# Kernel tuning notes

Measured on AMD Instinct MI355X. Metric: run time of the kernel, lower is better.

The kernel has to match this reference:

```python
import math
import jax, jax.numpy as jnp
import numpy as np

B, M, H, K, L = 8, 512, 512, 8, 1024  # batch, block, hidden, heads, span
D = H // K  # head_dim = 64; key/value length = M + L


def _skew(X):
    # shift every row one step right: [B', M, L] -> [B', M, M+L]
    Bp, Mm, Ll = X.shape
    X = jnp.pad(X, ((0, 0), (0, 0), (0, Mm + 1)))
    X = X.reshape(Bp, -1)[:, :-Mm]
    return X.reshape(Bp, Mm, Mm + Ll)


def _unskew(X):
    # reverse of _skew: [B', M, M+L] -> [B', M, L]
    Bp, Mm, Lt = X.shape
    Ll = Lt - Mm
    X = X.reshape(Bp, -1)
    X = jnp.pad(X, ((0, 0), (0, Mm)))
    X = X.reshape(Bp, Mm, Mm + Ll + 1)
    return X[:, :, :Ll]


def _heads(x):
    # [B, T, K*D] -> [B*K, T, D]
    b, t, _ = x.shape
    return x.reshape(b, t, K, D).transpose(0, 2, 1, 3).reshape(b * K, t, D)


def setup_inputs() -> dict:
    key0 = jax.random.key(0)
    ks = jax.random.split(key0, 8)
    s = 1.0 / math.sqrt(H)
    return {
        "query": jax.random.normal(ks[0], (B, M, H), jnp.float32),
        "key": jax.random.normal(ks[1], (B, M + L, H), jnp.float32),
        "value": jax.random.normal(ks[2], (B, M + L, H), jnp.float32),
        "key_pe": jax.random.normal(ks[3], (1, D, L), jnp.float32),
        "Wq": jax.random.normal(ks[4], (H, H), jnp.float32) * s,
        "Wk": jax.random.normal(ks[5], (H, H), jnp.float32) * s,
        "Wv": jax.random.normal(ks[6], (H, H), jnp.float32) * s,
        "Wo": jax.random.normal(ks[7], (H, H), jnp.float32) * s,
    }


def reference(query, key, value, key_pe, Wq, Wk, Wv, Wo):
    q = _heads(query @ Wq.T)   # [B*K, M, D]
    k = _heads(key @ Wk.T)     # [B*K, M+L, D]
    v = _heads(value @ Wv.T)   # [B*K, M+L, D]

    attn_cont = jnp.einsum('bmd,bnd->bmn', q, k)       # [B*K, M, M+L]
    attn_cont = _unskew(attn_cont)                      # [B*K, M, L]
    attn_pos = jnp.einsum('bmd,dl->bml', q, key_pe[0])  # [B*K, M, L]
    attn = jax.nn.softmax((attn_cont + attn_pos) / math.sqrt(D), axis=-1)

    attn_sk = _skew(attn)                               # [B*K, M, M+L]
    out = jnp.einsum('bmn,bnd->bmd', attn_sk, v)        # [B*K, M, D]
    out = out.reshape(B, K, M, D).transpose(0, 2, 1, 3).reshape(B, M, K * D)
    return out @ Wo.T
```

## Files before the change

### kernel.cpp

```cpp
#include <hip/hip_runtime.h>
#include <hip/hip_bf16.h>
#include <cstddef>
#include <math.h>


#define HDIM 512
#define MQ 512
#define NK 1536
#define LSPAN 1024
#define SHIFT 5.0f

typedef _Float16 f16_t;
typedef f16_t f16x8 __attribute__((ext_vector_type(8)));
typedef f16_t f16x4 __attribute__((ext_vector_type(4)));
typedef float f32x4 __attribute__((ext_vector_type(4)));

#define MFMA16F(a, b, c) __builtin_amdgcn_mfma_f32_16x16x32_f16((a), (b), (c), 0, 0, 0)

__device__ __forceinline__ void async_cp16(const void* g, void* l) {
  __builtin_amdgcn_global_load_lds((const __attribute__((address_space(1))) void*)g,
                                   (__attribute__((address_space(3))) void*)l, 16, 0, 0);
}

__global__ void cvt_qkv(const float* __restrict__ q, const float* __restrict__ k,
                        const float* __restrict__ v, f16_t* __restrict__ q16,
                        f16_t* __restrict__ k16, f16_t* __restrict__ v16) {
  int y = blockIdx.y;
  const float* s = (y == 0) ? q : (y == 1) ? k : v;
  f16_t* d = (y == 0) ? q16 : (y == 1) ? k16 : v16;
  int n4 = (y == 0) ? 524288 : 1572864;
  int i = blockIdx.x * 256 + threadIdx.x;
  if (i >= n4) return;
  float4 x = ((const float4*)s)[i];
  f16x4 o;
  o[0] = (f16_t)x.x; o[1] = (f16_t)x.y; o[2] = (f16_t)x.z; o[3] = (f16_t)x.w;
  ((f16x4*)d)[i] = o;
}

__global__ void prep_w(const float* __restrict__ Wq, const float* __restrict__ Wk,
                       const float* __restrict__ Wv, const float* __restrict__ Wo,
                       const float* __restrict__ pe,
                       f16_t* __restrict__ wq, f16_t* __restrict__ wk,
                       f16_t* __restrict__ wv, f16_t* __restrict__ wo,
                       f16_t* __restrict__ pet) {
  int i = blockIdx.x * 256 + threadIdx.x;
  if (i < 262144) {
    int seg = i >> 16, j = i & 65535;
    const float* s = (seg == 0) ? Wq : (seg == 1) ? Wk : (seg == 2) ? Wv : Wo;
    f16_t* d = (seg == 0) ? wq : (seg == 1) ? wk : (seg == 2) ? wv : wo;
    float4 x = ((const float4*)s)[j];
    f16x4 o;
    o[0] = (f16_t)x.x; o[1] = (f16_t)x.y; o[2] = (f16_t)x.z; o[3] = (f16_t)x.w;
    ((f16x4*)d)[j] = o;
  } else {
    int j = i - 262144;
    pet[(j & 1023) * 64 + (j >> 10)] = (f16_t)pe[j];
  }
}

__global__ __launch_bounds__(256) void gemm3(
    const f16_t* __restrict__ q16, const f16_t* __restrict__ k16, const f16_t* __restrict__ v16,
    const f16_t* __restrict__ wq, const f16_t* __restrict__ wk, const f16_t* __restrict__ wv,
    f16_t* __restrict__ qo, f16_t* __restrict__ ko, f16_t* __restrict__ vT) {
  __shared__ alignas(16) f16_t As[128 * 64];
  __shared__ alignas(16) f16_t Bs[128 * 64];

  const int bx = blockIdx.x;
  const f16_t *A, *Bm;
  f16_t* C;
  int row0, col0, ldc;
  if (bx < 128) {
    int t = bx;
    A = q16; Bm = wq; C = qo; ldc = HDIM;
    row0 = (t >> 2) * 128; col0 = (t & 3) * 128;
  } else if (bx < 512) {
    int t = bx - 128;
    A = k16; Bm = wk; C = ko; ldc = HDIM;
    row0 = (t >> 2) * 128; col0 = (t & 3) * 128;
  } else {
    int t = bx - 512;
    int b = t / 48, u = t % 48;
    A = wv; Bm = v16 + (size_t)b * NK * HDIM;
    C = vT + (size_t)b * 512 * NK; ldc = NK;
    row0 = (u / 12) * 128; col0 = (u % 12) * 128;
  }

  const int tid = threadIdx.x;
  const int lane = tid & 63, wave = tid >> 6;
  const int quad = lane >> 4, l16 = lane & 15;
  const int wr = (wave & 1) * 64, wc = (wave >> 1) * 64;
  const int rstage = tid >> 3, cstage = tid & 7;

  f32x4 acc[4][4] = {};
  for (int k0 = 0; k0 < HDIM; k0 += 64) {
#pragma unroll
    for (int i = 0; i < 4; ++i) {
      int r = i * 32 + rstage;
      int csw = cstage ^ (r & 7);
      async_cp16(A  + (size_t)(row0 + r) * HDIM + k0 + csw * 8, &As[i * 2048 + wave * 512]);
      async_cp16(Bm + (size_t)(col0 + r) * HDIM + k0 + csw * 8, &Bs[i * 2048 + wave * 512]);
    }
    __syncthreads();
#pragma unroll
    for (int ks = 0; ks < 2; ++ks) {
      f16x8 af[4], bf[4];
#pragma unroll
      for (int i = 0; i < 4; ++i) {
        int rA = wr + i * 16 + l16;
        af[i] = *(const f16x8*)&As[rA * 64 + (((ks * 4 + quad) ^ (rA & 7)) * 8)];
        int rB = wc + i * 16 + l16;
        bf[i] = *(const f16x8*)&Bs[rB * 64 + (((ks * 4 + quad) ^ (rB & 7)) * 8)];
      }
#pragma unroll
      for (int i = 0; i < 4; ++i)
#pragma unroll
        for (int n = 0; n < 4; ++n)
          acc[i][n] = MFMA16F(af[i], bf[n], acc[i][n]);
    }
    __syncthreads();
  }
#pragma unroll
  for (int i = 0; i < 4; ++i)
#pragma unroll
    for (int n = 0; n < 4; ++n)
#pragma unroll
      for (int r = 0; r < 4; ++r)
        C[(size_t)(row0 + wr + i * 16 + quad * 4 + r) * ldc + col0 + wc + n * 16 + l16] =
            (f16_t)acc[i][n][r];
}

__global__ __launch_bounds__(256) void attn2(const f16_t* __restrict__ q,
                                             const f16_t* __restrict__ k,
                                             const f16_t* __restrict__ vT,
                                             const f16_t* __restrict__ pet,
                                             f16_t* __restrict__ Opart,
                                             float* __restrict__ Lpart) {
  __shared__ alignas(16) f16_t Ks[2][4096];
  __shared__ alignas(16) f16_t Vs[4096];
  __shared__ alignas(16) f16_t Tst[4][128][20];
  __shared__ alignas(16) f16_t Ps[4][16][72];

  const int m0 = blockIdx.x * 64;
  const int bh = blockIdx.y;
  const int b = bh >> 3, kh = bh & 7;
  const int z = blockIdx.z;
  const int j0 = z ? 9 : 0, j1 = z ? 16 : 8;
  const int tid = threadIdx.x;
  const int lane = tid & 63, wave = tid >> 6;
  const int quad = lane >> 4, l16 = lane & 15;
  const int sr = wave * 16;
  const int rstage = tid >> 3, cstage = tid & 7;

  f16_t (*Tw)[20] = Tst[wave];
  f16_t (*Pw)[72] = Ps[wave];

  f16x8 qa0, qa1;
  {
    const f16_t* qrow = q + (size_t)(b * MQ + m0 + sr + l16) * HDIM + kh * 64;
    qa0 = *(const f16x8*)(qrow + quad * 8);
    qa1 = *(const f16x8*)(qrow + 32 + quad * 8);
#pragma unroll
    for (int e = 0; e < 8; ++e) {
      qa0[e] = (f16_t)((float)qa0[e] * 0.125f);
      qa1[e] = (f16_t)((float)qa1[e] * 0.125f);
    }
  }

  f16x8 ones;
#pragma unroll
  for (int e = 0; e < 8; ++e) ones[e] = (f16_t)1.0f;

  f32x4 oacc[4] = {};
  f32x4 lacc = {};

  const f16_t* kbh = k + (size_t)b * NK * HDIM + kh * 64;
  const f16_t* vbh = vT + (size_t)(b * 512 + kh * 64) * NK;

  if (z) {
#pragma unroll
    for (int ch = 0; ch < 4; ++ch) {
      int l = 512 + ch * 16 + l16;
      f16x8 s0 = *(const f16x8*)(pet + (size_t)l * 64 + quad * 8);
      f16x8 s1 = *(const f16x8*)(pet + (size_t)l * 64 + 32 + quad * 8);
      f32x4 tt = {};
      tt = MFMA16F(qa0, s0, tt);
      tt = MFMA16F(qa1, s1, tt);
      int sb = l + sr + quad * 4;
#pragma unroll
      for (int r = 0; r < 4; ++r)
        Tw[(sb + r) & 127][quad * 4 + r] = (f16_t)tt[r];
    }
  }

#pragma unroll
  for (int i = 0; i < 2; ++i) {
    int r = i * 32 + rstage;
    int nsrc = m0 + j0 * 64 + r;
    int csw = cstage ^ (r & 7);
    async_cp16(kbh + (size_t)nsrc * HDIM + csw * 8, &Ks[0][i * 2048 + wave * 512]);
  }

  int buf = 0;
  for (int j = j0; j <= j1; ++j, buf ^= 1) {
    __syncthreads();

    f16x8 pb0[4], pb1[4];
    if (j < 16) {
#pragma unroll
      for (int ch = 0; ch < 4; ++ch) {
        int l = j * 64 + ch * 16 + l16;
        pb0[ch] = *(const f16x8*)(pet + (size_t)l * 64 + quad * 8);
        pb1[ch] = *(const f16x8*)(pet + (size_t)l * 64 + 32 + quad * 8);
      }
    }
    {
      int ncol0 = m0 + j * 64;
#pragma unroll
      for (int i = 0; i < 2; ++i) {
        int d = i * 32 + rstage;
        int csw = cstage ^ (d & 7);
        async_cp16(vbh + (size_t)d * NK + ncol0 + csw * 8, &Vs[i * 2048 + wave * 512]);
      }
#pragma unroll
      for (int i = 0; i < 2; ++i) {
        int r = i * 32 + rstage;
        int nsrc = m0 + (j + 1) * 64 + r;
        nsrc = (nsrc < NK) ? nsrc : (NK - 1);
        int csw = cstage ^ (r & 7);
        async_cp16(kbh + (size_t)nsrc * HDIM + csw * 8, &Ks[buf ^ 1][i * 2048 + wave * 512]);
      }
    }
    if (j < 16) {
      const int l0 = j * 64;
#pragma unroll
      for (int ch = 0; ch < 4; ++ch) {
        f32x4 tt = {};
        tt = MFMA16F(qa0, pb0[ch], tt);
        tt = MFMA16F(qa1, pb1[ch], tt);
        int sb = l0 + ch * 16 + l16 + sr + quad * 4;
#pragma unroll
        for (int r = 0; r < 4; ++r)
          Tw[(sb + r) & 127][quad * 4 + r] = (f16_t)tt[r];
      }
    }
    f32x4 sacc[4];
#pragma unroll
    for (int ch = 0; ch < 4; ++ch) {
      int n = ch * 16 + l16;
      const f16_t* kr = &Ks[buf][n * 64];
      f16x8 kb0 = *(const f16x8*)&kr[(quad ^ (n & 7)) * 8];
      f16x8 kb1 = *(const f16x8*)&kr[((quad + 4) ^ (n & 7)) * 8];
      f32x4 s = {};
      s = MFMA16F(qa0, kb0, s);
      s = MFMA16F(qa1, kb1, s);
      sacc[ch] = s;
    }
#pragma unroll
    for (int ch = 0; ch < 4; ++ch) {
      int scol = (j * 64 + ch * 16 + l16) & 127;
      f16x4 tq = *(const f16x4*)&Tw[scol][quad * 4];
#pragma unroll
      for (int r = 0; r < 4; ++r) {
        int il = quad * 4 + r;
        int l = j * 64 + ch * 16 + l16 - sr - il;
        float pe_ = __expf(sacc[ch][r] + (float)tq[r] - SHIFT);
        float pv = (l >= 0 && l < LSPAN) ? pe_ : 0.f;
        Pw[il][ch * 16 + l16] = (f16_t)pv;
      }
    }
    f16x8 pa0 = *(const f16x8*)&Pw[l16][quad * 8];
    f16x8 pa1 = *(const f16x8*)&Pw[l16][32 + quad * 8];
    __builtin_amdgcn_s_waitcnt(0x0F72);
#pragma unroll
    for (int dch = 0; dch < 4; ++dch) {
      int d = dch * 16 + l16;
      const f16_t* vr = &Vs[d * 64];
      f16x8 vb0 = *(const f16x8*)&vr[(quad ^ (d & 7)) * 8];
      f16x8 vb1 = *(const f16x8*)&vr[((quad + 4) ^ (d & 7)) * 8];
      oacc[dch] = MFMA16F(pa0, vb0, oacc[dch]);
      oacc[dch] = MFMA16F(pa1, vb1, oacc[dch]);
    }
    lacc = MFMA16F(pa0, ones, lacc);
    lacc = MFMA16F(pa1, ones, lacc);
  }

  f16_t* Op = Opart + (size_t)z * 2097152;
#pragma unroll
  for (int r = 0; r < 4; ++r) {
    float inv = 1.0f / lacc[r];
    int m = m0 + sr + quad * 4 + r;
#pragma unroll
    for (int dch = 0; dch < 4; ++dch)
      Op[(size_t)(b * MQ + m) * HDIM + kh * 64 + dch * 16 + l16] =
          (f16_t)(oacc[dch][r] * inv);
    if (l16 == 0)
      Lpart[z * 32768 + bh * MQ + m] = lacc[r];
  }
}

__global__ __launch_bounds__(256) void gemm_wo(const f16_t* __restrict__ O0,
                                               const f16_t* __restrict__ O1,
                                               const float* __restrict__ Lpart,
                                               const f16_t* __restrict__ Bw,
                                               float* __restrict__ C) {
  __shared__ alignas(16) f16_t As[128][72];
  __shared__ alignas(16) f16_t Bs[64 * 64];
  const int bx = blockIdx.x;
  const int row0 = (bx >> 3) * 128, col0 = (bx & 7) * 64;
  const int tid = threadIdx.x;
  const int lane = tid & 63, wave = tid >> 6;
  const int quad = lane >> 4, l16 = lane & 15;
  const int wr = (wave & 1) * 64, wc = (wave >> 1) * 32;
  const int rstage = tid >> 3, cstage = tid & 7;
  const int cA8 = (tid & 7) * 8;

  f32x4 acc[4][2] = {};
  for (int k0 = 0; k0 < HDIM; k0 += 64) {
#pragma unroll
    for (int i = 0; i < 2; ++i) {
      int r = i * 32 + rstage;
      int csw = cstage ^ (r & 7);
      async_cp16(Bw + (size_t)(col0 + r) * HDIM + k0 + csw * 8, &Bs[i * 2048 + wave * 512]);
    }
#pragma unroll
    for (int i = 0; i < 4; ++i) {
      int r = i * 32 + rstage;
      int rg = row0 + r;
      int bb = rg >> 9, m = rg & 511;
      int head = (k0 + cA8) >> 6;
      int li = (bb * 8 + head) * MQ + m;
      float l0 = Lpart[li], l1 = Lpart[32768 + li];
      float w0 = l0 / (l0 + l1), w1 = 1.0f - w0;
      f16x8 o0 = *(const f16x8*)(O0 + (size_t)rg * HDIM + k0 + cA8);
      f16x8 o1 = *(const f16x8*)(O1 + (size_t)rg * HDIM + k0 + cA8);
      f16x8 a8;
#pragma unroll
      for (int e = 0; e < 8; ++e)
        a8[e] = (f16_t)((float)o0[e] * w0 + (float)o1[e] * w1);
      *(f16x8*)&As[r][cA8] = a8;
    }
    __syncthreads();
#pragma unroll
    for (int ks = 0; ks < 2; ++ks) {
      f16x8 af[4], bf[2];
#pragma unroll
      for (int i = 0; i < 4; ++i)
        af[i] = *(const f16x8*)&As[wr + i * 16 + l16][(ks * 4 + quad) * 8];
#pragma unroll
      for (int n = 0; n < 2; ++n) {
        int rB = wc + n * 16 + l16;
        bf[n] = *(const f16x8*)&Bs[rB * 64 + (((ks * 4 + quad) ^ (rB & 7)) * 8)];
      }
#pragma unroll
      for (int i = 0; i < 4; ++i)
#pragma unroll
        for (int n = 0; n < 2; ++n)
          acc[i][n] = MFMA16F(af[i], bf[n], acc[i][n]);
    }
    __syncthreads();
  }
#pragma unroll
  for (int i = 0; i < 4; ++i)
#pragma unroll
    for (int n = 0; n < 2; ++n)
#pragma unroll
      for (int r = 0; r < 4; ++r)
        C[(size_t)(row0 + wr + i * 16 + quad * 4 + r) * HDIM + col0 + wc + n * 16 + l16] =
            acc[i][n][r];
}

extern "C" void kernel_launch(void* const* d_in, const int* in_sizes, int n_in,
                              void* d_out, int out_size, void* d_ws, size_t ws_size,
                              hipStream_t stream) {
  const float* query  = (const float*)d_in[0];
  const float* key    = (const float*)d_in[1];
  const float* value  = (const float*)d_in[2];
  const float* key_pe = (const float*)d_in[3];
  const float* Wq     = (const float*)d_in[4];
  const float* Wk     = (const float*)d_in[5];
  const float* Wv     = (const float*)d_in[6];
  const float* Wo     = (const float*)d_in[7];
  float* out = (float*)d_out;

  f16_t* ws = (f16_t*)d_ws;
  f16_t* q16a = ws;
  f16_t* k16a = q16a + 2097152;
  f16_t* v16a = k16a + 6291456;
  f16_t* wq16 = v16a + 6291456;
  f16_t* wk16 = wq16 + 262144;
  f16_t* wv16 = wk16 + 262144;
  f16_t* wo16 = wv16 + 262144;
  f16_t* pet  = wo16 + 262144;
  f16_t* qo   = pet + 65536;
  f16_t* ko   = qo + 2097152;
  f16_t* vTo  = ko + 6291456;
  f16_t* Opart = k16a;
  float* Lpart = (float*)v16a;

  hipLaunchKernelGGL(cvt_qkv, dim3(6144, 3), dim3(256), 0, stream,
                     query, key, value, q16a, k16a, v16a);
  hipLaunchKernelGGL(prep_w, dim3(1280), dim3(256), 0, stream,
                     Wq, Wk, Wv, Wo, key_pe, wq16, wk16, wv16, wo16, pet);
  hipLaunchKernelGGL(gemm3, dim3(896), dim3(256), 0, stream,
                     q16a, k16a, v16a, wq16, wk16, wv16, qo, ko, vTo);
  hipLaunchKernelGGL(attn2, dim3(8, 64, 2), dim3(256), 0, stream,
                     qo, ko, vTo, pet, Opart, Lpart);
  hipLaunchKernelGGL(gemm_wo, dim3(256), dim3(256), 0, stream,
                     Opart, Opart + 2097152, Lpart, wo16, out);
}
```

Baseline: 214.5 us.

## Double-buffer projection GEMMs and merge conversion kernels into one launch

```diff
diff --git a/kernel.cpp b/kernel.cpp
--- a/kernel.cpp
+++ b/kernel.cpp
@@ -22,39 +22,40 @@
                                    (__attribute__((address_space(3))) void*)l, 16, 0, 0);
 }
 
-__global__ void cvt_qkv(const float* __restrict__ q, const float* __restrict__ k,
-                        const float* __restrict__ v, f16_t* __restrict__ q16,
-                        f16_t* __restrict__ k16, f16_t* __restrict__ v16) {
+__global__ void prep_all(const float* __restrict__ q, const float* __restrict__ k,
+                         const float* __restrict__ v,
+                         const float* __restrict__ Wq, const float* __restrict__ Wk,
+                         const float* __restrict__ Wv, const float* __restrict__ Wo,
+                         const float* __restrict__ pe,
+                         f16_t* __restrict__ q16, f16_t* __restrict__ k16,
+                         f16_t* __restrict__ v16,
+                         f16_t* __restrict__ wq, f16_t* __restrict__ wk,
+                         f16_t* __restrict__ wv, f16_t* __restrict__ wo,
+                         f16_t* __restrict__ pet) {
   int y = blockIdx.y;
-  const float* s = (y == 0) ? q : (y == 1) ? k : v;
-  f16_t* d = (y == 0) ? q16 : (y == 1) ? k16 : v16;
-  int n4 = (y == 0) ? 524288 : 1572864;
   int i = blockIdx.x * 256 + threadIdx.x;
-  if (i >= n4) return;
-  float4 x = ((const float4*)s)[i];
-  f16x4 o;
-  o[0] = (f16_t)x.x; o[1] = (f16_t)x.y; o[2] = (f16_t)x.z; o[3] = (f16_t)x.w;
-  ((f16x4*)d)[i] = o;
-}
-
-__global__ void prep_w(const float* __restrict__ Wq, const float* __restrict__ Wk,
-                       const float* __restrict__ Wv, const float* __restrict__ Wo,
-                       const float* __restrict__ pe,
-                       f16_t* __restrict__ wq, f16_t* __restrict__ wk,
-                       f16_t* __restrict__ wv, f16_t* __restrict__ wo,
-                       f16_t* __restrict__ pet) {
-  int i = blockIdx.x * 256 + threadIdx.x;
-  if (i < 262144) {
-    int seg = i >> 16, j = i & 65535;
-    const float* s = (seg == 0) ? Wq : (seg == 1) ? Wk : (seg == 2) ? Wv : Wo;
-    f16_t* d = (seg == 0) ? wq : (seg == 1) ? wk : (seg == 2) ? wv : wo;
-    float4 x = ((const float4*)s)[j];
+  if (y < 3) {
+    const float* s = (y == 0) ? q : (y == 1) ? k : v;
+    f16_t* d = (y == 0) ? q16 : (y == 1) ? k16 : v16;
+    int n4 = (y == 0) ? 524288 : 1572864;
+    if (i >= n4) return;
+    float4 x = ((const float4*)s)[i];
     f16x4 o;
     o[0] = (f16_t)x.x; o[1] = (f16_t)x.y; o[2] = (f16_t)x.z; o[3] = (f16_t)x.w;
-    ((f16x4*)d)[j] = o;
+    ((f16x4*)d)[i] = o;
   } else {
-    int j = i - 262144;
-    pet[(j & 1023) * 64 + (j >> 10)] = (f16_t)pe[j];
+    if (i < 262144) {
+      int seg = i >> 16, j = i & 65535;
+      const float* s = (seg == 0) ? Wq : (seg == 1) ? Wk : (seg == 2) ? Wv : Wo;
+      f16_t* d = (seg == 0) ? wq : (seg == 1) ? wk : (seg == 2) ? wv : wo;
+      float4 x = ((const float4*)s)[j];
+      f16x4 o;
+      o[0] = (f16_t)x.x; o[1] = (f16_t)x.y; o[2] = (f16_t)x.z; o[3] = (f16_t)x.w;
+      ((f16x4*)d)[j] = o;
+    } else if (i < 327680) {
+      int j = i - 262144;
+      pet[(j & 1023) * 64 + (j >> 10)] = (f16_t)pe[j];
+    }
   }
 }
 
@@ -62,8 +63,8 @@
     const f16_t* __restrict__ q16, const f16_t* __restrict__ k16, const f16_t* __restrict__ v16,
     const f16_t* __restrict__ wq, const f16_t* __restrict__ wk, const f16_t* __restrict__ wv,
     f16_t* __restrict__ qo, f16_t* __restrict__ ko, f16_t* __restrict__ vT) {
-  __shared__ alignas(16) f16_t As[128 * 64];
-  __shared__ alignas(16) f16_t Bs[128 * 64];
+  __shared__ alignas(16) f16_t As[2][8192];
+  __shared__ alignas(16) f16_t Bs[2][8192];
 
   const int bx = blockIdx.x;
   const f16_t *A, *Bm;
@@ -91,25 +92,39 @@
   const int wr = (wave & 1) * 64, wc = (wave >> 1) * 64;
   const int rstage = tid >> 3, cstage = tid & 7;
 
+#pragma unroll
+  for (int i = 0; i < 4; ++i) {
+    int r = i * 32 + rstage;
+    int csw = cstage ^ (r & 7);
+    async_cp16(A  + (size_t)(row0 + r) * HDIM + csw * 8, &As[0][i * 2048 + wave * 512]);
+    async_cp16(Bm + (size_t)(col0 + r) * HDIM + csw * 8, &Bs[0][i * 2048 + wave * 512]);
+  }
+
   f32x4 acc[4][4] = {};
-  for (int k0 = 0; k0 < HDIM; k0 += 64) {
-#pragma unroll
-    for (int i = 0; i < 4; ++i) {
-      int r = i * 32 + rstage;
-      int csw = cstage ^ (r & 7);
-      async_cp16(A  + (size_t)(row0 + r) * HDIM + k0 + csw * 8, &As[i * 2048 + wave * 512]);
-      async_cp16(Bm + (size_t)(col0 + r) * HDIM + k0 + csw * 8, &Bs[i * 2048 + wave * 512]);
-    }
+  for (int it = 0; it < 8; ++it) {
+    const int buf = it & 1;
     __syncthreads();
+    if (it + 1 < 8) {
+      int k0 = (it + 1) * 64;
+#pragma unroll
+      for (int i = 0; i < 4; ++i) {
+        int r = i * 32 + rstage;
+        int csw = cstage ^ (r & 7);
+        async_cp16(A  + (size_t)(row0 + r) * HDIM + k0 + csw * 8,
+                   &As[buf ^ 1][i * 2048 + wave * 512]);
+        async_cp16(Bm + (size_t)(col0 + r) * HDIM + k0 + csw * 8,
+                   &Bs[buf ^ 1][i * 2048 + wave * 512]);
+      }
+    }
 #pragma unroll
     for (int ks = 0; ks < 2; ++ks) {
       f16x8 af[4], bf[4];
 #pragma unroll
       for (int i = 0; i < 4; ++i) {
         int rA = wr + i * 16 + l16;
-        af[i] = *(const f16x8*)&As[rA * 64 + (((ks * 4 + quad) ^ (rA & 7)) * 8)];
+        af[i] = *(const f16x8*)&As[buf][rA * 64 + (((ks * 4 + quad) ^ (rA & 7)) * 8)];
         int rB = wc + i * 16 + l16;
-        bf[i] = *(const f16x8*)&Bs[rB * 64 + (((ks * 4 + quad) ^ (rB & 7)) * 8)];
+        bf[i] = *(const f16x8*)&Bs[buf][rB * 64 + (((ks * 4 + quad) ^ (rB & 7)) * 8)];
       }
 #pragma unroll
       for (int i = 0; i < 4; ++i)
@@ -117,7 +132,6 @@
         for (int n = 0; n < 4; ++n)
           acc[i][n] = MFMA16F(af[i], bf[n], acc[i][n]);
     }
-    __syncthreads();
   }
 #pragma unroll
   for (int i = 0; i < 4; ++i)
@@ -303,8 +317,8 @@
                                                const float* __restrict__ Lpart,
                                                const f16_t* __restrict__ Bw,
                                                float* __restrict__ C) {
-  __shared__ alignas(16) f16_t As[128][72];
-  __shared__ alignas(16) f16_t Bs[64 * 64];
+  __shared__ alignas(16) f16_t As[2][128][72];
+  __shared__ alignas(16) f16_t Bs[2][4096];
   const int bx = blockIdx.x;
   const int row0 = (bx >> 3) * 128, col0 = (bx & 7) * 64;
   const int tid = threadIdx.x;
@@ -314,21 +328,14 @@
   const int rstage = tid >> 3, cstage = tid & 7;
   const int cA8 = (tid & 7) * 8;
 
-  f32x4 acc[4][2] = {};
-  for (int k0 = 0; k0 < HDIM; k0 += 64) {
-#pragma unroll
-    for (int i = 0; i < 2; ++i) {
-      int r = i * 32 + rstage;
-      int csw = cstage ^ (r & 7);
-      async_cp16(Bw + (size_t)(col0 + r) * HDIM + k0 + csw * 8, &Bs[i * 2048 + wave * 512]);
-    }
+  f16x8 areg[4];
+  auto loadA = [&](int it) {
+    int k0 = it * 64;
+    int head = (k0 + cA8) >> 6;
 #pragma unroll
     for (int i = 0; i < 4; ++i) {
-      int r = i * 32 + rstage;
-      int rg = row0 + r;
-      int bb = rg >> 9, m = rg & 511;
-      int head = (k0 + cA8) >> 6;
-      int li = (bb * 8 + head) * MQ + m;
+      int rg = row0 + i * 32 + rstage;
+      int li = ((rg >> 9) * 8 + head) * MQ + (rg & 511);
       float l0 = Lpart[li], l1 = Lpart[32768 + li];
       float w0 = l0 / (l0 + l1), w1 = 1.0f - w0;
       f16x8 o0 = *(const f16x8*)(O0 + (size_t)rg * HDIM + k0 + cA8);
@@ -337,19 +344,46 @@
 #pragma unroll
       for (int e = 0; e < 8; ++e)
         a8[e] = (f16_t)((float)o0[e] * w0 + (float)o1[e] * w1);
-      *(f16x8*)&As[r][cA8] = a8;
-    }
+      areg[i] = a8;
+    }
+  };
+
+  loadA(0);
+#pragma unroll
+  for (int i = 0; i < 2; ++i) {
+    int r = i * 32 + rstage;
+    int csw = cstage ^ (r & 7);
+    async_cp16(Bw + (size_t)(col0 + r) * HDIM + csw * 8, &Bs[0][i * 2048 + wave * 512]);
+  }
+#pragma unroll
+  for (int i = 0; i < 4; ++i)
+    *(f16x8*)&As[0][i * 32 + rstage][cA8] = areg[i];
+
+  f32x4 acc[4][2] = {};
+  for (int it = 0; it < 8; ++it) {
+    const int buf = it & 1;
     __syncthreads();
+    if (it + 1 < 8) {
+      int k0 = (it + 1) * 64;
+#pragma unroll
+      for (int i = 0; i < 2; ++i) {
+        int r = i * 32 + rstage;
+        int csw = cstage ^ (r & 7);
+        async_cp16(Bw + (size_t)(col0 + r) * HDIM + k0 + csw * 8,
+                   &Bs[buf ^ 1][i * 2048 + wave * 512]);
+      }
+      loadA(it + 1);
+    }
 #pragma unroll
     for (int ks = 0; ks < 2; ++ks) {
       f16x8 af[4], bf[2];
 #pragma unroll
       for (int i = 0; i < 4; ++i)
-        af[i] = *(const f16x8*)&As[wr + i * 16 + l16][(ks * 4 + quad) * 8];
+        af[i] = *(const f16x8*)&As[buf][wr + i * 16 + l16][(ks * 4 + quad) * 8];
 #pragma unroll
       for (int n = 0; n < 2; ++n) {
         int rB = wc + n * 16 + l16;
-        bf[n] = *(const f16x8*)&Bs[rB * 64 + (((ks * 4 + quad) ^ (rB & 7)) * 8)];
+        bf[n] = *(const f16x8*)&Bs[buf][rB * 64 + (((ks * 4 + quad) ^ (rB & 7)) * 8)];
       }
 #pragma unroll
       for (int i = 0; i < 4; ++i)
@@ -357,7 +391,11 @@
         for (int n = 0; n < 2; ++n)
           acc[i][n] = MFMA16F(af[i], bf[n], acc[i][n]);
     }
-    __syncthreads();
+    if (it + 1 < 8) {
+#pragma unroll
+      for (int i = 0; i < 4; ++i)
+        *(f16x8*)&As[buf ^ 1][i * 32 + rstage][cA8] = areg[i];
+    }
   }
 #pragma unroll
   for (int i = 0; i < 4; ++i)
@@ -397,10 +435,9 @@
   f16_t* Opart = k16a;
   float* Lpart = (float*)v16a;
 
-  hipLaunchKernelGGL(cvt_qkv, dim3(6144, 3), dim3(256), 0, stream,
-                     query, key, value, q16a, k16a, v16a);
-  hipLaunchKernelGGL(prep_w, dim3(1280), dim3(256), 0, stream,
-                     Wq, Wk, Wv, Wo, key_pe, wq16, wk16, wv16, wo16, pet);
+  hipLaunchKernelGGL(prep_all, dim3(6144, 4), dim3(256), 0, stream,
+                     query, key, value, Wq, Wk, Wv, Wo, key_pe,
+                     q16a, k16a, v16a, wq16, wk16, wv16, wo16, pet);
   hipLaunchKernelGGL(gemm3, dim3(896), dim3(256), 0, stream,
                      q16a, k16a, v16a, wq16, wk16, wv16, qo, ko, vTo);
   hipLaunchKernelGGL(attn2, dim3(8, 64, 2), dim3(256), 0, stream,
```

After: 210.3 us. 1.02x faster.
